# Kernel tuning notes

Hardware: AMD Instinct MI355X
Metric: run time of the kernel (lower is better)

Reference implementation:

```python
import jax, jax.numpy as jnp
import numpy as np
from jax import lax

N, R, W, H = 256, 32, 8, 6       # batch, n_rooms, room width/height
MX, MY = 72, 72                  # map grid
EMB = 6                          # room embedding width
CIN = 10 + EMB                   # conv input channels


def _boundaries(m):
    # m: [R, W, H] binary room masks -> [R, 4, W, H] (left, right, up, down edges)
    left = jnp.concatenate([m[:, :1, :], jnp.clip(m[:, 1:, :] - m[:, :-1, :], 0)], axis=1)
    right = jnp.concatenate([jnp.clip(m[:, :-1, :] - m[:, 1:, :], 0), m[:, -1:, :]], axis=1)
    up = jnp.concatenate([m[:, :, :1], jnp.clip(m[:, :, 1:] - m[:, :, :-1], 0)], axis=2)
    down = jnp.concatenate([jnp.clip(m[:, :, :-1] - m[:, :, 1:], 0), m[:, :, -1:]], axis=2)
    return jnp.stack([left, right, up, down], axis=1)


def setup_inputs() -> dict:
    key = jax.random.key(0)
    ks = jax.random.split(key, 12)
    room_map = (jax.random.uniform(ks[0], (R, W, H)) < 0.7).astype(jnp.float32)
    room_map = room_map.at[:, 0, 0].set(1.0)  # guarantee nonempty rooms
    doors = (jax.random.uniform(ks[1], (R, 4, W, H)) < 0.15).astype(jnp.float32) * room_map[:, None]
    room_tensor = jnp.concatenate([room_map[:, None], doors, _boundaries(room_map)], axis=1)  # [R,9,W,H]
    px = jax.random.randint(ks[2], (N, R), 0, MX - W)
    py = jax.random.randint(ks[3], (N, R), 0, MY - H)
    room_positions = jnp.stack([px, py], axis=-1).astype(jnp.int32)  # [N,R,2]

    def rn(k, shape, fan_in):
        return jax.random.normal(k, shape, jnp.float32) / np.float32(np.sqrt(fan_in))

    inp = dict(room_positions=room_positions, room_tensor=room_tensor)
    inp['room_embedding'] = jax.random.normal(ks[4], (R, EMB), jnp.float32)
    inp['w_conv1'] = rn(ks[5], (64, CIN, 5, 5), CIN * 25); inp['b_conv1'] = jnp.zeros((64,), jnp.float32)
    inp['w_conv2'] = rn(ks[6], (64, 64, 3, 3), 64 * 9);    inp['b_conv2'] = jnp.zeros((64,), jnp.float32)
    inp['w_conv3'] = rn(ks[7], (64, 64, 3, 3), 64 * 9);    inp['b_conv3'] = jnp.zeros((64,), jnp.float32)
    inp['w_room1'] = rn(ks[8], (128, 64), 64);   inp['b_room1'] = jnp.zeros((128,), jnp.float32)
    inp['w_room2'] = rn(ks[9], (128, 128), 128); inp['b_room2'] = jnp.zeros((128,), jnp.float32)
    inp['w_fc1'] = rn(ks[10], (256, 128), 128);  inp['b_fc1'] = jnp.zeros((256,), jnp.float32)
    inp['w_fc2'] = rn(ks[11], (256, 256), 256);  inp['b_fc2'] = jnp.zeros((256,), jnp.float32)
    return inp


def _conv2d_relu(x, w, b):
    pad = w.shape[-1] // 2
    y = lax.conv_general_dilated(x, w, (1, 1), [(pad, pad), (pad, pad)],
                                 dimension_numbers=('NCHW', 'OIHW', 'NCHW'))
    return jax.nn.relu(y + b[None, :, None, None])


def _forward(room_positions, room_tensor, room_embedding,
             w_conv1, b_conv1, w_conv2, b_conv2, w_conv3, b_conv3,
             w_room1, b_room1, w_room2, b_room2, w_fc1, b_fc1, w_fc2, b_fc2):
    room_map = room_tensor[:, 0]                      # [R,W,H]
    px = room_positions[..., 0]                       # [N,R]
    py = room_positions[..., 1]
    # ---- encode_map: scatter-add all rooms into grid ----
    bidx = jnp.arange(N)[:, None, None, None, None]
    cidx = jnp.arange(9)[None, None, :, None, None]
    ix = px[:, :, None, None, None] + jnp.arange(W)[None, None, None, :, None]   # [N,R,1,W,1]
    iy = py[:, :, None, None, None] + jnp.arange(H)[None, None, None, None, :]   # [N,R,1,1,H]
    map9 = jnp.zeros((N, 9, MX, MY), jnp.float32).at[bidx, cidx, ix, iy].add(room_tensor[None])
    eidx = jnp.arange(EMB)[None, None, :, None, None]
    evals = room_embedding[:, :, None, None] * room_map[:, None, :, :]           # [R,EMB,W,H]
    embg = jnp.zeros((N, EMB, MX, MY), jnp.float32).at[bidx, eidx, ix, iy].add(evals[None])
    X = jnp.concatenate([map9, jnp.ones((N, 1, MX, MY), jnp.float32), embg], axis=1)  # [N,16,MX,MY]
    # ---- map convs ----
    X = _conv2d_relu(X, w_conv1, b_conv1)
    X = _conv2d_relu(X, w_conv2, b_conv2)
    X = _conv2d_relu(X, w_conv3, b_conv3)
    # ---- decode_map: gather room tiles, masked mean per room ----
    Xt = jnp.transpose(X, (0, 2, 3, 1))                                          # [N,MX,MY,C]
    g = Xt[jnp.arange(N)[:, None, None, None],
           px[:, :, None, None] + jnp.arange(W)[None, None, :, None],
           py[:, :, None, None] + jnp.arange(H)[None, None, None, :]]            # [N,R,W,H,C]
    g = g * room_map[None, :, :, :, None]
    room_feat = g.sum(axis=(2, 3)) / room_map.sum(axis=(1, 2))[None, :, None]    # [N,R,C]
    X = jnp.transpose(room_feat, (0, 2, 1))                                      # [N,C,R]
    # ---- 1x1 conv1d room layers ----
    X = jax.nn.relu(jnp.einsum('ncr,oc->nor', X, w_room1) + b_room1[None, :, None])
    X = jax.nn.relu(jnp.einsum('ncr,oc->nor', X, w_room2) + b_room2[None, :, None])
    # ---- fc head: sum over rooms, MLP ----
    X = X.sum(axis=2)                                                            # [N,128]
    X = jax.nn.relu(X @ w_fc1.T + b_fc1)
    return X @ w_fc2.T + b_fc2                                                   # [N,256]


def reference(room_positions, room_tensor, room_embedding,
              w_conv1, b_conv1, w_conv2, b_conv2, w_conv3, b_conv3,
              w_room1, b_room1, w_room2, b_room2, w_fc1, b_fc1, w_fc2, b_fc2):
    return _forward(room_positions, room_tensor, room_embedding,
                    w_conv1, b_conv1, w_conv2, b_conv2, w_conv3, b_conv3,
                    w_room1, b_room1, w_room2, b_room2, w_fc1, b_fc1, w_fc2, b_fc2)
```

## Files before the change

### kernel.cpp

```cpp
#include <hip/hip_runtime.h>
#include <hip/hip_bf16.h>
#include <cstddef>

#define NB 256
#define RR 32
#define WW 8
#define HH 6
#define MXY 72
#define EMB 6
#define CIN1 16

typedef __bf16 bf16x8 __attribute__((ext_vector_type(8)));
typedef float floatx4 __attribute__((ext_vector_type(4)));

static const size_t B_W1F  = 0;
static const size_t B_W2F  = 57344;
static const size_t B_W3F  = 131072;
static const size_t B_RAUX = 204800;
static const size_t B_RINV = 205056;
static const size_t B_HEAD = 205312;
static const size_t F_WR1T = 0;
static const size_t F_WR2T = 8192;
static const size_t F_F1T  = 24576;
static const size_t F_F2T  = 57344;
static const size_t B_FEAT = 696832;
static const size_t B_IMSK = 2793984;
static const size_t B_SSUM = 2826752;

__device__ inline short f2b(float f) {
    unsigned u = __builtin_bit_cast(unsigned, f);
    unsigned r = (u + 0x7fffu + ((u >> 16) & 1u)) >> 16;
    return (short)r;
}

__global__ void prep_all(const float* __restrict__ w1, const float* __restrict__ w2,
                         const float* __restrict__ w3, const float* __restrict__ wr1,
                         const float* __restrict__ wr2, const float* __restrict__ wf1,
                         const float* __restrict__ wf2, const float* __restrict__ rt,
                         const int* __restrict__ pos, char* __restrict__ ws)
{
    short* W1F = (short*)(ws + B_W1F);
    short* W2F = (short*)(ws + B_W2F);
    short* W3F = (short*)(ws + B_W3F);
    float* HEAD = (float*)(ws + B_HEAD);

    int idx = blockIdx.x * 256 + threadIdx.x;
    if (idx < 28672) {
        int j = idx & 7, lane = (idx >> 3) & 63, nt = (idx >> 9) & 3, kk = idx >> 11;
        int k = kk * 32 + (lane >> 4) * 8 + j;
        int oc = nt * 16 + (lane & 15);
        int tap = k >> 4, ci = k & 15;
        float v = (tap < 25) ? w1[(oc * 16 + ci) * 25 + tap] : 0.f;
        W1F[idx] = f2b(v);
        return;
    }
    idx -= 28672;
    if (idx < 36864) {
        int j = idx & 7, lane = (idx >> 3) & 63, nt = (idx >> 9) & 3, kk = idx >> 11;
        int k = kk * 32 + (lane >> 4) * 8 + j;
        int oc = nt * 16 + (lane & 15);
        int tap = k >> 6, cp = k & 63;
        int ci = (cp >> 2) + (cp & 3) * 16;
        W2F[idx] = f2b(w2[(oc * 64 + ci) * 9 + tap]);
        return;
    }
    idx -= 36864;
    if (idx < 36864) {
        int j = idx & 7, lane = (idx >> 3) & 63, nt = (idx >> 9) & 3, kk = idx >> 11;
        int k = kk * 32 + (lane >> 4) * 8 + j;
        int oc = nt * 16 + (lane & 15);
        int tap = k >> 6, cp = k & 63;
        int ci = (cp >> 2) + (cp & 3) * 16;
        W3F[idx] = f2b(w3[(oc * 64 + ci) * 9 + tap]);
        return;
    }
    idx -= 36864;
    if (idx < 8192)  { int o = idx & 127, c = idx >> 7; HEAD[F_WR1T + idx] = wr1[o * 64 + c]; return; }
    idx -= 8192;
    if (idx < 16384) { int o = idx & 127, c = idx >> 7; HEAD[F_WR2T + idx] = wr2[o * 128 + c]; return; }
    idx -= 16384;
    if (idx < 32768) { int o = idx & 255, c = idx >> 8; HEAD[F_F1T + idx] = wf1[o * 128 + c]; return; }
    idx -= 32768;
    if (idx < 65536) { int o = idx & 255, c = idx >> 8; HEAD[F_F2T + idx] = wf2[o * 256 + c]; return; }
    idx -= 65536;
    if (idx < 8192) {
        const int n = idx >> 5, r0 = idx & 31;
        const int px0 = pos[(n * RR + r0) * 2 + 0];
        const int py0 = pos[(n * RR + r0) * 2 + 1];
        unsigned m = 0;
        for (int r = 0; r < RR; ++r) {
            int rpx = pos[(n * RR + r) * 2 + 0];
            int rpy = pos[(n * RR + r) * 2 + 1];
            if (rpx >= px0 - 11 && rpx <= px0 + 11 && rpy >= py0 - 9 && rpy <= py0 + 9)
                m |= 1u << r;
        }
        ((unsigned*)(ws + B_IMSK))[n * RR + r0] = m;
        return;
    }
    idx -= 8192;
    if (idx < RR) {
        unsigned long long m = 0ull;
        int cnt = 0;
        for (int j = 0; j < WW * HH; ++j)
            if (rt[idx * 9 * 48 + j] != 0.f) { m |= (1ull << j); ++cnt; }
        ((unsigned long long*)(ws + B_RAUX))[idx] = m;
        ((float*)(ws + B_RINV))[idx] = 1.f / (float)cnt;
    }
}

__global__ __launch_bounds__(256, 4) void fused_conv(
    const unsigned* __restrict__ imask, const float* __restrict__ rt,
    const float* __restrict__ emb, const short* __restrict__ wAll,
    const float* __restrict__ bc1, const float* __restrict__ bc2,
    const float* __restrict__ bc3, const int* __restrict__ pos,
    const unsigned long long* __restrict__ rmask, float* __restrict__ feat)
{
    __shared__ __align__(16) short s_Y1[120 * 72];
    __shared__ __align__(16) short s_u[80 * 72];
    __shared__ float s_feat[64];

    const int tid = threadIdx.x;
    const int lane = tid & 63;
    const int wv = tid >> 6;
    const int ml = lane & 15;
    const int q = lane >> 4;
    const int room = blockIdx.x;
    const int n = blockIdx.y;

    const int px = pos[(n * RR + room) * 2 + 0];
    const int py = pos[(n * RR + room) * 2 + 1];

    const short* W1F = wAll;
    const short* W2F = wAll + B_W2F / 2;
    const short* W3F = wAll + B_W3F / 2;

    bf16x8 Bb[2][4];
    auto load_k = [&](const short* wF, int kk, bf16x8* dst) {
        const short* src = wF + (size_t)kk * 2048;
#pragma unroll
        for (int j2 = 0; j2 < 4; ++j2)
            dst[j2] = *reinterpret_cast<const bf16x8*>(src + (j2 * 64 + lane) * 8);
    };

    load_k(W1F, 0, Bb[0]);

    {
        const unsigned mk0 = imask[n * RR + room];
        if (tid < 224) {
            const int row = tid / 14, col = tid - (tid / 14) * 14;
            const int gx = px - 4 + row, gy = py - 4 + col;
            float a[16];
#pragma unroll
            for (int c = 0; c < 16; ++c) a[c] = 0.f;
            a[9] = ((unsigned)gx < (unsigned)MXY && (unsigned)gy < (unsigned)MXY) ? 1.f : 0.f;

            unsigned mm = mk0;
            while (mm) {
                const int r = __builtin_ctz(mm);
                mm &= mm - 1;
                const int rpx = pos[(n * RR + r) * 2 + 0];
                const int rpy = pos[(n * RR + r) * 2 + 1];
                const int w = gx - rpx, h = gy - rpy;
                if ((unsigned)w < (unsigned)WW && (unsigned)h < (unsigned)HH) {
                    const int j = w * HH + h;
                    const float* rr = rt + r * 9 * 48;
#pragma unroll
                    for (int c = 0; c < 9; ++c) a[c] += rr[c * 48 + j];
                    const float mv = rr[j];
#pragma unroll
                    for (int e = 0; e < EMB; ++e) a[10 + e] += emb[r * EMB + e] * mv;
                }
            }
            short o[16];
#pragma unroll
            for (int c = 0; c < 16; ++c) o[c] = f2b(a[c]);
            *reinterpret_cast<uint4*>(&s_u[tid * 24 + 0]) = *reinterpret_cast<uint4*>(o);
            *reinterpret_cast<uint4*>(&s_u[tid * 24 + 8]) = *reinterpret_cast<uint4*>(o + 8);
        }
    }
    __syncthreads();

    {
        int prow[2], pcol[2];
#pragma unroll
        for (int i = 0; i < 2; ++i) {
            int p = wv * 32 + i * 16 + ml;
            if (p > 119) p = 119;
            prow[i] = p / 10; pcol[i] = p - prow[i] * 10;
        }
        floatx4 acc1[2][4] = {};

#pragma unroll
        for (int kk = 0; kk < 13; ++kk) {
            if (kk < 12) load_k(W1F, kk + 1, Bb[(kk + 1) & 1]);
            else         load_k(W2F, 0, Bb[1]);
            int tap = kk * 2 + (q >> 1);
            if (tap > 24) tap = 24;
            int chb = (q & 1) * 8;
            int dx = tap / 5, dy = tap - dx * 5;
            __builtin_amdgcn_s_setprio(1);
#pragma unroll
            for (int i = 0; i < 2; ++i) {
                bf16x8 A = *reinterpret_cast<const bf16x8*>(
                    &s_u[((prow[i] + dx) * 14 + (pcol[i] + dy)) * 24 + chb]);
#pragma unroll
                for (int j2 = 0; j2 < 4; ++j2)
                    acc1[i][j2] = __builtin_amdgcn_mfma_f32_16x16x32_bf16(
                        A, Bb[kk & 1][j2], acc1[i][j2], 0, 0, 0);
            }
            __builtin_amdgcn_s_setprio(0);
        }
        float b4[4];
#pragma unroll
        for (int j2 = 0; j2 < 4; ++j2) b4[j2] = bc1[j2 * 16 + ml];
#pragma unroll
        for (int i = 0; i < 2; ++i)
#pragma unroll
            for (int r = 0; r < 4; ++r) {
                int p = wv * 32 + i * 16 + q * 4 + r;
                if (p < 120) {
                    unsigned lo = (unsigned)(unsigned short)f2b(fmaxf(acc1[i][0][r] + b4[0], 0.f))
                                | ((unsigned)(unsigned short)f2b(fmaxf(acc1[i][1][r] + b4[1], 0.f)) << 16);
                    unsigned hi = (unsigned)(unsigned short)f2b(fmaxf(acc1[i][2][r] + b4[2], 0.f))
                                | ((unsigned)(unsigned short)f2b(fmaxf(acc1[i][3][r] + b4[3], 0.f)) << 16);
                    *reinterpret_cast<uint2*>(&s_Y1[p * 72 + ml * 4]) = make_uint2(lo, hi);
                }
            }
    }
    __syncthreads();

    {
        int prowA, pcolA, prowB, pcolB;
        {
            int p0 = wv * 16 + ml; prowA = p0 >> 3; pcolA = p0 & 7;
            int p1 = 64 + ml;      prowB = p1 >> 3; pcolB = p1 & 7;
        }
        floatx4 acc2[4] = {};
        floatx4 acc2s = {};

#pragma unroll
        for (int kk = 0; kk < 18; ++kk) {
            if (kk < 17) load_k(W2F, kk + 1, Bb[kk & 1]);
            else         load_k(W3F, 0, Bb[1]);
            bf16x8 B4 = *reinterpret_cast<const bf16x8*>(
                W2F + (size_t)kk * 2048 + (wv * 64 + lane) * 8);
            const int tap = kk >> 1;
            const int chb = (kk & 1) * 32 + q * 8;
            const int dx = tap / 3, dy = tap - (tap / 3) * 3;
            bf16x8 A0 = *reinterpret_cast<const bf16x8*>(
                &s_Y1[((prowA + dx) * 10 + (pcolA + dy)) * 72 + chb]);
            bf16x8 A4 = *reinterpret_cast<const bf16x8*>(
                &s_Y1[((prowB + dx) * 10 + (pcolB + dy)) * 72 + chb]);
            __builtin_amdgcn_s_setprio(1);
#pragma unroll
            for (int j2 = 0; j2 < 4; ++j2)
                acc2[j2] = __builtin_amdgcn_mfma_f32_16x16x32_bf16(A0, Bb[(kk + 1) & 1][j2], acc2[j2], 0, 0, 0);
            acc2s = __builtin_amdgcn_mfma_f32_16x16x32_bf16(A4, B4, acc2s, 0, 0, 0);
            __builtin_amdgcn_s_setprio(0);
        }
        float b4[4];
#pragma unroll
        for (int j2 = 0; j2 < 4; ++j2) b4[j2] = bc2[j2 * 16 + ml];
#pragma unroll
        for (int r = 0; r < 4; ++r) {
            int p = wv * 16 + q * 4 + r;
            unsigned lo = (unsigned)(unsigned short)f2b(fmaxf(acc2[0][r] + b4[0], 0.f))
                        | ((unsigned)(unsigned short)f2b(fmaxf(acc2[1][r] + b4[1], 0.f)) << 16);
            unsigned hi = (unsigned)(unsigned short)f2b(fmaxf(acc2[2][r] + b4[2], 0.f))
                        | ((unsigned)(unsigned short)f2b(fmaxf(acc2[3][r] + b4[3], 0.f)) << 16);
            *reinterpret_cast<uint2*>(&s_u[p * 72 + ml * 4]) = make_uint2(lo, hi);
        }
        {
            float bt = bc2[wv * 16 + ml];
#pragma unroll
            for (int r = 0; r < 4; ++r) {
                int p = 64 + q * 4 + r;
                s_u[p * 72 + ml * 4 + wv] = f2b(fmaxf(acc2s[r] + bt, 0.f));
            }
        }
        if (tid < 64) s_feat[tid] = 0.f;
    }
    __syncthreads();

    if (wv < 3) {
        int p0 = wv * 16 + ml;
        int row3 = p0 / 6, col3 = p0 - (p0 / 6) * 6;
        floatx4 acc3[4] = {};

#pragma unroll
        for (int kk = 0; kk < 18; ++kk) {
            if (kk < 17) load_k(W3F, kk + 1, Bb[kk & 1]);
            const int tap = kk >> 1;
            const int chb = (kk & 1) * 32 + q * 8;
            const int dx = tap / 3, dy = tap - (tap / 3) * 3;
            bf16x8 A = *reinterpret_cast<const bf16x8*>(
                &s_u[((row3 + dx) * 8 + (col3 + dy)) * 72 + chb]);
            __builtin_amdgcn_s_setprio(1);
#pragma unroll
            for (int j2 = 0; j2 < 4; ++j2)
                acc3[j2] = __builtin_amdgcn_mfma_f32_16x16x32_bf16(A, Bb[(kk + 1) & 1][j2], acc3[j2], 0, 0, 0);
            __builtin_amdgcn_s_setprio(0);
        }
        float b4[4];
#pragma unroll
        for (int j2 = 0; j2 < 4; ++j2) b4[j2] = bc3[j2 * 16 + ml];
        float part[4] = {0.f, 0.f, 0.f, 0.f};
        const unsigned long long mk = rmask[room];
#pragma unroll
        for (int r = 0; r < 4; ++r) {
            int p = wv * 16 + q * 4 + r;
            if ((mk >> p) & 1ull) {
#pragma unroll
                for (int j2 = 0; j2 < 4; ++j2)
                    part[j2] += fmaxf(acc3[j2][r] + b4[j2], 0.f);
            }
        }
#pragma unroll
        for (int j2 = 0; j2 < 4; ++j2) {
            part[j2] += __shfl_xor(part[j2], 16);
            part[j2] += __shfl_xor(part[j2], 32);
        }
        if (q == 0) {
#pragma unroll
            for (int j2 = 0; j2 < 4; ++j2)
                atomicAdd(&s_feat[j2 * 16 + ml], part[j2]);
        }
    }
    __syncthreads();
    if (tid < 64)
        feat[((size_t)n * RR + room) * 64 + tid] = s_feat[tid];
}

__global__ __launch_bounds__(256) void head_rooms(const float* __restrict__ feat,
                                                  const float* __restrict__ HEAD,
                                                  const float* __restrict__ rinv,
                                                  const float* __restrict__ b1,
                                                  const float* __restrict__ b2,
                                                  float* __restrict__ ssum)
{
    __shared__ __align__(16) float s_feat[8 * 64];
    __shared__ __align__(16) float s_h1[8 * 128];
    __shared__ __align__(16) float s_s[2 * 128];

    const int qr = blockIdx.x;
    const int n = blockIdx.y;
    const int tid = threadIdx.x;
    const float* W1t = HEAD + F_WR1T;
    const float* W2t = HEAD + F_WR2T;

    for (int i = tid; i < 8 * 64; i += 256)
        s_feat[i] = feat[(size_t)n * RR * 64 + qr * 512 + i] * rinv[qr * 8 + (i >> 6)];
    __syncthreads();

    const int o = tid & 127;
    const int rh = tid >> 7;

    float acc[4];
#pragma unroll
    for (int r = 0; r < 4; ++r) acc[r] = b1[o];
    for (int c4 = 0; c4 < 16; ++c4) {
        float w0 = W1t[(c4 * 4 + 0) * 128 + o];
        float w1 = W1t[(c4 * 4 + 1) * 128 + o];
        float w2 = W1t[(c4 * 4 + 2) * 128 + o];
        float w3 = W1t[(c4 * 4 + 3) * 128 + o];
#pragma unroll
        for (int r = 0; r < 4; ++r) {
            float4 f = *reinterpret_cast<const float4*>(&s_feat[(rh * 4 + r) * 64 + c4 * 4]);
            acc[r] += f.x * w0 + f.y * w1 + f.z * w2 + f.w * w3;
        }
    }
#pragma unroll
    for (int r = 0; r < 4; ++r) s_h1[(rh * 4 + r) * 128 + o] = fmaxf(acc[r], 0.f);
    __syncthreads();

#pragma unroll
    for (int r = 0; r < 4; ++r) acc[r] = b2[o];
    for (int c4 = 0; c4 < 32; ++c4) {
        float w0 = W2t[(c4 * 4 + 0) * 128 + o];
        float w1 = W2t[(c4 * 4 + 1) * 128 + o];
        float w2 = W2t[(c4 * 4 + 2) * 128 + o];
        float w3 = W2t[(c4 * 4 + 3) * 128 + o];
#pragma unroll
        for (int r = 0; r < 4; ++r) {
            float4 f = *reinterpret_cast<const float4*>(&s_h1[(rh * 4 + r) * 128 + c4 * 4]);
            acc[r] += f.x * w0 + f.y * w1 + f.z * w2 + f.w * w3;
        }
    }
    float ps = 0.f;
#pragma unroll
    for (int r = 0; r < 4; ++r) ps += fmaxf(acc[r], 0.f);
    s_s[rh * 128 + o] = ps;
    __syncthreads();
    if (tid < 128)
        ssum[((size_t)n * 4 + qr) * 128 + tid] = s_s[tid] + s_s[128 + tid];
}

__global__ __launch_bounds__(256) void head_fc(const float* __restrict__ ssum,
                                               const float* __restrict__ HEAD,
                                               const float* __restrict__ bf1,
                                               const float* __restrict__ bf2,
                                               float* __restrict__ outp)
{
    __shared__ __align__(16) float s_sf[128];
    __shared__ __align__(16) float s_t1[256];

    const int n = blockIdx.x;
    const int tid = threadIdx.x;
    const float* F1t = HEAD + F_F1T;
    const float* F2t = HEAD + F_F2T;

    if (tid < 128) {
        const float* s0 = ssum + (size_t)n * 4 * 128 + tid;
        s_sf[tid] = (s0[0] + s0[128]) + (s0[256] + s0[384]);
    }
    __syncthreads();

    {
        float a = bf1[tid];
#pragma unroll 4
        for (int c4 = 0; c4 < 32; ++c4) {
            float4 f = *reinterpret_cast<const float4*>(&s_sf[c4 * 4]);
            a += f.x * F1t[(c4 * 4 + 0) * 256 + tid];
            a += f.y * F1t[(c4 * 4 + 1) * 256 + tid];
            a += f.z * F1t[(c4 * 4 + 2) * 256 + tid];
            a += f.w * F1t[(c4 * 4 + 3) * 256 + tid];
        }
        s_t1[tid] = fmaxf(a, 0.f);
    }
    __syncthreads();

    {
        float a = bf2[tid];
#pragma unroll 4
        for (int c4 = 0; c4 < 64; ++c4) {
            float4 f = *reinterpret_cast<const float4*>(&s_t1[c4 * 4]);
            a += f.x * F2t[(c4 * 4 + 0) * 256 + tid];
            a += f.y * F2t[(c4 * 4 + 1) * 256 + tid];
            a += f.z * F2t[(c4 * 4 + 2) * 256 + tid];
            a += f.w * F2t[(c4 * 4 + 3) * 256 + tid];
        }
        outp[(size_t)n * 256 + tid] = a;
    }
}

extern "C" void kernel_launch(void* const* d_in, const int* in_sizes, int n_in,
                              void* d_out, int out_size, void* d_ws, size_t ws_size,
                              hipStream_t stream)
{
    const int* pos = (const int*)d_in[0];
    const float* rt = (const float*)d_in[1];
    const float* emb = (const float*)d_in[2];
    const float* w1 = (const float*)d_in[3];
    const float* bc1 = (const float*)d_in[4];
    const float* w2 = (const float*)d_in[5];
    const float* bc2 = (const float*)d_in[6];
    const float* w3 = (const float*)d_in[7];
    const float* bc3 = (const float*)d_in[8];
    const float* wr1 = (const float*)d_in[9];
    const float* br1 = (const float*)d_in[10];
    const float* wr2 = (const float*)d_in[11];
    const float* br2 = (const float*)d_in[12];
    const float* wf1 = (const float*)d_in[13];
    const float* bf1 = (const float*)d_in[14];
    const float* wf2 = (const float*)d_in[15];
    const float* bf2 = (const float*)d_in[16];
    float* out = (float*)d_out;
    char* ws = (char*)d_ws;

    prep_all<<<913, 256, 0, stream>>>(w1, w2, w3, wr1, wr2, wf1, wf2, rt, pos, ws);

    const short* WALL = (const short*)(ws + B_W1F);
    const unsigned long long* RMASK = (const unsigned long long*)(ws + B_RAUX);
    const float* RINV = (const float*)(ws + B_RINV);
    const float* HEAD = (const float*)(ws + B_HEAD);
    float* FEAT = (float*)(ws + B_FEAT);
    unsigned* IMSK = (unsigned*)(ws + B_IMSK);
    float* SSUM = (float*)(ws + B_SSUM);

    fused_conv<<<dim3(RR, NB), 256, 0, stream>>>(IMSK, rt, emb, WALL,
                                                 bc1, bc2, bc3, pos, RMASK, FEAT);

    head_rooms<<<dim3(4, NB), 256, 0, stream>>>(FEAT, HEAD, RINV, br1, br2, SSUM);
    head_fc<<<NB, 256, 0, stream>>>(SSUM, HEAD, bf1, bf2, out);
}
```

Measured before the change: 300.7 us.

## Stage conv weights in LDS via global_load_lds double buffering

Each wave used to fetch every weight slice from global memory into its own registers. Now the block stages the conv weights into a double-buffered LDS area with asynchronous global_load_lds, two k-slices per phase, and every wave reads its B fragments from LDS. This removes the four-fold redundant global and L1 weight traffic. In exchange it adds a block-wide barrier every phase (about 25 in total) and 16 KB more LDS, and lowers the launch-bounds occupancy hint from 4 to 3.

```diff
diff --git a/kernel.cpp b/kernel.cpp
--- a/kernel.cpp
+++ b/kernel.cpp
@@ -108,7 +108,7 @@
     }
 }
 
-__global__ __launch_bounds__(256, 4) void fused_conv(
+__global__ __launch_bounds__(256, 3) void fused_conv(
     const unsigned* __restrict__ imask, const float* __restrict__ rt,
     const float* __restrict__ emb, const short* __restrict__ wAll,
     const float* __restrict__ bc1, const float* __restrict__ bc2,
@@ -117,6 +117,7 @@
 {
     __shared__ __align__(16) short s_Y1[120 * 72];
     __shared__ __align__(16) short s_u[80 * 72];
+    __shared__ __align__(16) short s_B[2][4096];
     __shared__ float s_feat[64];
 
     const int tid = threadIdx.x;
@@ -130,19 +131,19 @@
     const int px = pos[(n * RR + room) * 2 + 0];
     const int py = pos[(n * RR + room) * 2 + 1];
 
-    const short* W1F = wAll;
-    const short* W2F = wAll + B_W2F / 2;
-    const short* W3F = wAll + B_W3F / 2;
-
-    bf16x8 Bb[2][4];
-    auto load_k = [&](const short* wF, int kk, bf16x8* dst) {
-        const short* src = wF + (size_t)kk * 2048;
-#pragma unroll
-        for (int j2 = 0; j2 < 4; ++j2)
-            dst[j2] = *reinterpret_cast<const bf16x8*>(src + (j2 * 64 + lane) * 8);
+    const char* wB = (const char*)wAll;
+    auto dma = [&](int ph) {
+        const char* src = wB + (size_t)ph * 8192 + wv * 2048 + lane * 16;
+        short* d0 = &s_B[ph & 1][wv * 1024];
+        __builtin_amdgcn_global_load_lds(
+            (const __attribute__((address_space(1))) unsigned int*)src,
+            (__attribute__((address_space(3))) unsigned int*)d0, 16, 0, 0);
+        __builtin_amdgcn_global_load_lds(
+            (const __attribute__((address_space(1))) unsigned int*)(src + 1024),
+            (__attribute__((address_space(3))) unsigned int*)(d0 + 512), 16, 0, 0);
     };
 
-    load_k(W1F, 0, Bb[0]);
+    dma(0);
 
     {
         const unsigned mk0 = imask[n * RR + room];
@@ -191,43 +192,53 @@
         floatx4 acc1[2][4] = {};
 
 #pragma unroll
-        for (int kk = 0; kk < 13; ++kk) {
-            if (kk < 12) load_k(W1F, kk + 1, Bb[(kk + 1) & 1]);
-            else         load_k(W2F, 0, Bb[1]);
-            int tap = kk * 2 + (q >> 1);
-            if (tap > 24) tap = 24;
-            int chb = (q & 1) * 8;
-            int dx = tap / 5, dy = tap - dx * 5;
-            __builtin_amdgcn_s_setprio(1);
-#pragma unroll
-            for (int i = 0; i < 2; ++i) {
-                bf16x8 A = *reinterpret_cast<const bf16x8*>(
-                    &s_u[((prow[i] + dx) * 14 + (pcol[i] + dy)) * 24 + chb]);
+        for (int t = 0; t < 7; ++t) {
+            dma(t + 1);
+            const short* sb = s_B[t & 1];
+#pragma unroll
+            for (int kb = 0; kb < 2; ++kb) {
+                const int kk = t * 2 + kb;
+                bf16x8 Bf[4];
 #pragma unroll
                 for (int j2 = 0; j2 < 4; ++j2)
-                    acc1[i][j2] = __builtin_amdgcn_mfma_f32_16x16x32_bf16(
-                        A, Bb[kk & 1][j2], acc1[i][j2], 0, 0, 0);
-            }
-            __builtin_amdgcn_s_setprio(0);
-        }
-        float b4[4];
-#pragma unroll
-        for (int j2 = 0; j2 < 4; ++j2) b4[j2] = bc1[j2 * 16 + ml];
-#pragma unroll
-        for (int i = 0; i < 2; ++i)
-#pragma unroll
-            for (int r = 0; r < 4; ++r) {
-                int p = wv * 32 + i * 16 + q * 4 + r;
-                if (p < 120) {
-                    unsigned lo = (unsigned)(unsigned short)f2b(fmaxf(acc1[i][0][r] + b4[0], 0.f))
-                                | ((unsigned)(unsigned short)f2b(fmaxf(acc1[i][1][r] + b4[1], 0.f)) << 16);
-                    unsigned hi = (unsigned)(unsigned short)f2b(fmaxf(acc1[i][2][r] + b4[2], 0.f))
-                                | ((unsigned)(unsigned short)f2b(fmaxf(acc1[i][3][r] + b4[3], 0.f)) << 16);
-                    *reinterpret_cast<uint2*>(&s_Y1[p * 72 + ml * 4]) = make_uint2(lo, hi);
-                }
-            }
-    }
-    __syncthreads();
+                    Bf[j2] = *reinterpret_cast<const bf16x8*>(&sb[kb * 2048 + (j2 * 64 + lane) * 8]);
+                int tap = kk * 2 + (q >> 1);
+                if (tap > 24) tap = 24;
+                const int chb = (q & 1) * 8;
+                const int dx = tap / 5, dy = tap - (tap / 5) * 5;
+                __builtin_amdgcn_s_setprio(1);
+#pragma unroll
+                for (int i = 0; i < 2; ++i) {
+                    bf16x8 A = *reinterpret_cast<const bf16x8*>(
+                        &s_u[((prow[i] + dx) * 14 + (pcol[i] + dy)) * 24 + chb]);
+#pragma unroll
+                    for (int j2 = 0; j2 < 4; ++j2)
+                        acc1[i][j2] = __builtin_amdgcn_mfma_f32_16x16x32_bf16(
+                            A, Bf[j2], acc1[i][j2], 0, 0, 0);
+                }
+                __builtin_amdgcn_s_setprio(0);
+            }
+            if (t == 6) {
+                float b4[4];
+#pragma unroll
+                for (int j2 = 0; j2 < 4; ++j2) b4[j2] = bc1[j2 * 16 + ml];
+#pragma unroll
+                for (int i = 0; i < 2; ++i)
+#pragma unroll
+                    for (int r = 0; r < 4; ++r) {
+                        int p = wv * 32 + i * 16 + q * 4 + r;
+                        if (p < 120) {
+                            unsigned lo = (unsigned)(unsigned short)f2b(fmaxf(acc1[i][0][r] + b4[0], 0.f))
+                                        | ((unsigned)(unsigned short)f2b(fmaxf(acc1[i][1][r] + b4[1], 0.f)) << 16);
+                            unsigned hi = (unsigned)(unsigned short)f2b(fmaxf(acc1[i][2][r] + b4[2], 0.f))
+                                        | ((unsigned)(unsigned short)f2b(fmaxf(acc1[i][3][r] + b4[3], 0.f)) << 16);
+                            *reinterpret_cast<uint2*>(&s_Y1[p * 72 + ml * 4]) = make_uint2(lo, hi);
+                        }
+                    }
+            }
+            __syncthreads();
+        }
+    }
 
     {
         int prowA, pcolA, prowB, pcolB;
@@ -239,94 +250,118 @@
         floatx4 acc2s = {};
 
 #pragma unroll
-        for (int kk = 0; kk < 18; ++kk) {
-            if (kk < 17) load_k(W2F, kk + 1, Bb[kk & 1]);
-            else         load_k(W3F, 0, Bb[1]);
-            bf16x8 B4 = *reinterpret_cast<const bf16x8*>(
-                W2F + (size_t)kk * 2048 + (wv * 64 + lane) * 8);
-            const int tap = kk >> 1;
-            const int chb = (kk & 1) * 32 + q * 8;
-            const int dx = tap / 3, dy = tap - (tap / 3) * 3;
-            bf16x8 A0 = *reinterpret_cast<const bf16x8*>(
-                &s_Y1[((prowA + dx) * 10 + (pcolA + dy)) * 72 + chb]);
-            bf16x8 A4 = *reinterpret_cast<const bf16x8*>(
-                &s_Y1[((prowB + dx) * 10 + (pcolB + dy)) * 72 + chb]);
-            __builtin_amdgcn_s_setprio(1);
-#pragma unroll
-            for (int j2 = 0; j2 < 4; ++j2)
-                acc2[j2] = __builtin_amdgcn_mfma_f32_16x16x32_bf16(A0, Bb[(kk + 1) & 1][j2], acc2[j2], 0, 0, 0);
-            acc2s = __builtin_amdgcn_mfma_f32_16x16x32_bf16(A4, B4, acc2s, 0, 0, 0);
-            __builtin_amdgcn_s_setprio(0);
-        }
-        float b4[4];
-#pragma unroll
-        for (int j2 = 0; j2 < 4; ++j2) b4[j2] = bc2[j2 * 16 + ml];
-#pragma unroll
-        for (int r = 0; r < 4; ++r) {
-            int p = wv * 16 + q * 4 + r;
-            unsigned lo = (unsigned)(unsigned short)f2b(fmaxf(acc2[0][r] + b4[0], 0.f))
-                        | ((unsigned)(unsigned short)f2b(fmaxf(acc2[1][r] + b4[1], 0.f)) << 16);
-            unsigned hi = (unsigned)(unsigned short)f2b(fmaxf(acc2[2][r] + b4[2], 0.f))
-                        | ((unsigned)(unsigned short)f2b(fmaxf(acc2[3][r] + b4[3], 0.f)) << 16);
-            *reinterpret_cast<uint2*>(&s_u[p * 72 + ml * 4]) = make_uint2(lo, hi);
-        }
+        for (int t = 0; t < 9; ++t) {
+            dma(8 + t);
+            const short* sb = s_B[(7 + t) & 1];
+#pragma unroll
+            for (int kb = 0; kb < 2; ++kb) {
+                bf16x8 Bf[4];
+#pragma unroll
+                for (int j2 = 0; j2 < 4; ++j2)
+                    Bf[j2] = *reinterpret_cast<const bf16x8*>(&sb[kb * 2048 + (j2 * 64 + lane) * 8]);
+                bf16x8 B4 = *reinterpret_cast<const bf16x8*>(&sb[kb * 2048 + (wv * 64 + lane) * 8]);
+                const int kk = t * 2 + kb;
+                const int tap = kk >> 1;
+                const int chb = (kk & 1) * 32 + q * 8;
+                const int dx = tap / 3, dy = tap - (tap / 3) * 3;
+                bf16x8 A0 = *reinterpret_cast<const bf16x8*>(
+                    &s_Y1[((prowA + dx) * 10 + (pcolA + dy)) * 72 + chb]);
+                bf16x8 A4 = *reinterpret_cast<const bf16x8*>(
+                    &s_Y1[((prowB + dx) * 10 + (pcolB + dy)) * 72 + chb]);
+                __builtin_amdgcn_s_setprio(1);
+#pragma unroll
+                for (int j2 = 0; j2 < 4; ++j2)
+                    acc2[j2] = __builtin_amdgcn_mfma_f32_16x16x32_bf16(A0, Bf[j2], acc2[j2], 0, 0, 0);
+                acc2s = __builtin_amdgcn_mfma_f32_16x16x32_bf16(A4, B4, acc2s, 0, 0, 0);
+                __builtin_amdgcn_s_setprio(0);
+            }
+            if (t == 8) {
+                float b4[4];
+#pragma unroll
+                for (int j2 = 0; j2 < 4; ++j2) b4[j2] = bc2[j2 * 16 + ml];
+#pragma unroll
+                for (int r = 0; r < 4; ++r) {
+                    int p = wv * 16 + q * 4 + r;
+                    unsigned lo = (unsigned)(unsigned short)f2b(fmaxf(acc2[0][r] + b4[0], 0.f))
+                                | ((unsigned)(unsigned short)f2b(fmaxf(acc2[1][r] + b4[1], 0.f)) << 16);
+                    unsigned hi = (unsigned)(unsigned short)f2b(fmaxf(acc2[2][r] + b4[2], 0.f))
+                                | ((unsigned)(unsigned short)f2b(fmaxf(acc2[3][r] + b4[3], 0.f)) << 16);
+                    *reinterpret_cast<uint2*>(&s_u[p * 72 + ml * 4]) = make_uint2(lo, hi);
+                }
+                float bt = bc2[wv * 16 + ml];
+#pragma unroll
+                for (int r = 0; r < 4; ++r) {
+                    int p = 64 + q * 4 + r;
+                    s_u[p * 72 + ml * 4 + wv] = f2b(fmaxf(acc2s[r] + bt, 0.f));
+                }
+                if (tid < 64) s_feat[tid] = 0.f;
+            }
+            __syncthreads();
+        }
+    }
+
+    {
+        int prow3, pcol3;
         {
-            float bt = bc2[wv * 16 + ml];
-#pragma unroll
-            for (int r = 0; r < 4; ++r) {
-                int p = 64 + q * 4 + r;
-                s_u[p * 72 + ml * 4 + wv] = f2b(fmaxf(acc2s[r] + bt, 0.f));
-            }
-        }
-        if (tid < 64) s_feat[tid] = 0.f;
-    }
-    __syncthreads();
-
-    if (wv < 3) {
-        int p0 = wv * 16 + ml;
-        int row3 = p0 / 6, col3 = p0 - (p0 / 6) * 6;
+            int p0 = wv * 16 + ml;
+            prow3 = p0 / 6; pcol3 = p0 - (p0 / 6) * 6;
+        }
         floatx4 acc3[4] = {};
 
 #pragma unroll
-        for (int kk = 0; kk < 18; ++kk) {
-            if (kk < 17) load_k(W3F, kk + 1, Bb[kk & 1]);
-            const int tap = kk >> 1;
-            const int chb = (kk & 1) * 32 + q * 8;
-            const int dx = tap / 3, dy = tap - (tap / 3) * 3;
-            bf16x8 A = *reinterpret_cast<const bf16x8*>(
-                &s_u[((row3 + dx) * 8 + (col3 + dy)) * 72 + chb]);
-            __builtin_amdgcn_s_setprio(1);
-#pragma unroll
-            for (int j2 = 0; j2 < 4; ++j2)
-                acc3[j2] = __builtin_amdgcn_mfma_f32_16x16x32_bf16(A, Bb[(kk + 1) & 1][j2], acc3[j2], 0, 0, 0);
-            __builtin_amdgcn_s_setprio(0);
-        }
-        float b4[4];
-#pragma unroll
-        for (int j2 = 0; j2 < 4; ++j2) b4[j2] = bc3[j2 * 16 + ml];
-        float part[4] = {0.f, 0.f, 0.f, 0.f};
-        const unsigned long long mk = rmask[room];
-#pragma unroll
-        for (int r = 0; r < 4; ++r) {
-            int p = wv * 16 + q * 4 + r;
-            if ((mk >> p) & 1ull) {
-#pragma unroll
-                for (int j2 = 0; j2 < 4; ++j2)
-                    part[j2] += fmaxf(acc3[j2][r] + b4[j2], 0.f);
-            }
-        }
-#pragma unroll
-        for (int j2 = 0; j2 < 4; ++j2) {
-            part[j2] += __shfl_xor(part[j2], 16);
-            part[j2] += __shfl_xor(part[j2], 32);
-        }
-        if (q == 0) {
-#pragma unroll
-            for (int j2 = 0; j2 < 4; ++j2)
-                atomicAdd(&s_feat[j2 * 16 + ml], part[j2]);
-        }
-    }
-    __syncthreads();
+        for (int t = 0; t < 9; ++t) {
+            if (t < 8) dma(17 + t);
+            const short* sb = s_B[(16 + t) & 1];
+            if (wv < 3) {
+#pragma unroll
+                for (int kb = 0; kb < 2; ++kb) {
+                    const int kk = t * 2 + kb;
+                    bf16x8 Bf[4];
+#pragma unroll
+                    for (int j2 = 0; j2 < 4; ++j2)
+                        Bf[j2] = *reinterpret_cast<const bf16x8*>(&sb[kb * 2048 + (j2 * 64 + lane) * 8]);
+                    const int tap = kk >> 1;
+                    const int chb = (kk & 1) * 32 + q * 8;
+                    const int dx = tap / 3, dy = tap - (tap / 3) * 3;
+                    bf16x8 A = *reinterpret_cast<const bf16x8*>(
+                        &s_u[((prow3 + dx) * 8 + (pcol3 + dy)) * 72 + chb]);
+                    __builtin_amdgcn_s_setprio(1);
+#pragma unroll
+                    for (int j2 = 0; j2 < 4; ++j2)
+                        acc3[j2] = __builtin_amdgcn_mfma_f32_16x16x32_bf16(A, Bf[j2], acc3[j2], 0, 0, 0);
+                    __builtin_amdgcn_s_setprio(0);
+                }
+            }
+            if (t == 8 && wv < 3) {
+                float b4[4];
+#pragma unroll
+                for (int j2 = 0; j2 < 4; ++j2) b4[j2] = bc3[j2 * 16 + ml];
+                float part[4] = {0.f, 0.f, 0.f, 0.f};
+                const unsigned long long mk = rmask[room];
+#pragma unroll
+                for (int r = 0; r < 4; ++r) {
+                    int p = wv * 16 + q * 4 + r;
+                    if ((mk >> p) & 1ull) {
+#pragma unroll
+                        for (int j2 = 0; j2 < 4; ++j2)
+                            part[j2] += fmaxf(acc3[j2][r] + b4[j2], 0.f);
+                    }
+                }
+#pragma unroll
+                for (int j2 = 0; j2 < 4; ++j2) {
+                    part[j2] += __shfl_xor(part[j2], 16);
+                    part[j2] += __shfl_xor(part[j2], 32);
+                }
+                if (q == 0) {
+#pragma unroll
+                    for (int j2 = 0; j2 < 4; ++j2)
+                        atomicAdd(&s_feat[j2 * 16 + ml], part[j2]);
+                }
+            }
+            __syncthreads();
+        }
+    }
+
     if (tid < 64)
         feat[((size_t)n * RR + room) * 64 + tid] = s_feat[tid];
 }
```

Measured after the change: 277.1 us. 1.09x faster.
